# Kernel optimization log

Measured on AMD Instinct MI355X. Metric: run time of the kernel, lower is better.

## Reference

```python
import jax, jax.numpy as jnp
import numpy as np

B, C, HF, WF = 64, 512, 28, 28
HID = 512
NUM_CLS = 30
LOC_REG = 8
MAX_LEN = 500  # loop runs MAX_LEN + 1 = 501 steps


def setup_inputs() -> dict:
    key = jax.random.key(0)
    ks = jax.random.split(key, 12)
    sc = 0.02
    rn = lambda k, shape: jax.random.normal(k, shape, jnp.float32) * sc
    z = lambda shape: jnp.zeros(shape, jnp.float32)
    return {
        "fea": jax.random.normal(ks[0], (B, C, HF, WF), jnp.float32),
        # AttentionGRUCell params
        "i2h_w": rn(ks[1], (HID, C)),            # Linear(C, H, bias=False)
        "h2h_w": rn(ks[2], (HID, HID)),
        "h2h_b": z((HID,)),
        "score_w": rn(ks[3], (1, HID)),          # Linear(H, 1, bias=False)
        "gru_w_ih": rn(ks[4], (3 * HID, C + NUM_CLS)),
        "gru_w_hh": rn(ks[5], (3 * HID, HID)),
        "gru_b_ih": z((3 * HID,)),
        "gru_b_hh": z((3 * HID,)),
        # structure_generator: Linear(H,H) -> Linear(H, NUM_CLS) (no activation)
        "sg1_w": rn(ks[6], (HID, HID)), "sg1_b": z((HID,)),
        "sg2_w": rn(ks[7], (NUM_CLS, HID)), "sg2_b": z((NUM_CLS,)),
        # loc_generator: Linear(H,H) -> Linear(H, LOC_REG) -> Sigmoid
        "lg1_w": rn(ks[8], (HID, HID)), "lg1_b": z((HID,)),
        "lg2_w": rn(ks[9], (LOC_REG, HID)), "lg2_b": z((LOC_REG,)),
    }


def reference(fea, i2h_w, h2h_w, h2h_b, score_w, gru_w_ih, gru_w_hh,
              gru_b_ih, gru_b_hh, sg1_w, sg1_b, sg2_w, sg2_b,
              lg1_w, lg1_b, lg2_w, lg2_b):
    b = fea.shape[0]
    feat = fea.reshape(b, fea.shape[1], -1).transpose(0, 2, 1)      # [B, T, C]
    # i2h(batch_H) is step-invariant: hoist it out of the decode loop
    feat_proj = jnp.einsum('btc,hc->bth', feat, i2h_w)              # [B, T, H]
    sv = score_w[0]                                                  # [H]

    def gru_cell(x, h):
        gi = x @ gru_w_ih.T + gru_b_ih
        gh = h @ gru_w_hh.T + gru_b_hh
        i_r, i_z, i_n = jnp.split(gi, 3, axis=-1)
        h_r, h_z, h_n = jnp.split(gh, 3, axis=-1)
        r = jax.nn.sigmoid(i_r + h_r)
        z = jax.nn.sigmoid(i_z + h_z)
        n = jnp.tanh(i_n + r * h_n)
        return (1.0 - z) * n + z * h

    def step(carry, _):
        hidden, pre_chars = carry
        onehot = jax.nn.one_hot(pre_chars, NUM_CLS, dtype=feat.dtype)
        hproj = hidden @ h2h_w.T + h2h_b                             # [B, H]
        e = jnp.einsum('bth,h->bt', jnp.tanh(feat_proj + hproj[:, None, :]), sv)
        alpha = jax.nn.softmax(e, axis=1)                            # [B, T]
        context = jnp.einsum('bt,btc->bc', alpha, feat)              # [B, C]
        x = jnp.concatenate([context, onehot], axis=1)               # [B, C+NUM_CLS]
        new_hidden = gru_cell(x, hidden)
        structure_step = (new_hidden @ sg1_w.T + sg1_b) @ sg2_w.T + sg2_b
        loc_step = jax.nn.sigmoid((new_hidden @ lg1_w.T + lg1_b) @ lg2_w.T + lg2_b)
        new_chars = jnp.argmax(structure_step, axis=1)               # greedy decode
        return (new_hidden, new_chars), (structure_step, loc_step)

    hidden0 = jnp.zeros((b, HID), feat.dtype)
    chars0 = jnp.zeros((b,), jnp.int32)
    _, (structs, locs) = jax.lax.scan(step, (hidden0, chars0), None, length=MAX_LEN + 1)
    structure_probs = jax.nn.softmax(structs.transpose(1, 0, 2), axis=-1)  # eval-mode softmax
    loc_preds = locs.transpose(1, 0, 2)
    return structure_probs, loc_preds
```

## Files before the change

kernel.cpp:

```cpp
#include <hip/hip_runtime.h>
#include <hip/hip_bf16.h>


#define NB 64
#define TT 784
#define CC 512
#define HH 512
#define NCLS 30
#define LREG 8
#define STEPS 501
#define GRID_MAIN 256
#define THR_MAIN 1024

struct SlaP {
  __hip_bfloat16* feat16;
  __hip_bfloat16* fp16;
  float* hid2;
  float* hproj;
  float* h1sg;
  float* h1lg;
  float* ctx2;
  float* wsum;
  int*   chars;
  unsigned* bar;
  const float *score_w, *w_ih, *w_hh, *b_ih, *b_hh;
  const float *h2h_w, *h2h_b, *sg1_w, *sg1_b, *sg2_w, *sg2_b;
  const float *lg1_w, *lg1_b, *lg2_w, *lg2_b;
  float *out_probs, *out_loc;
};

__device__ __forceinline__ float lo16(unsigned v){ return __uint_as_float(v << 16); }
__device__ __forceinline__ float hi16(unsigned v){ return __uint_as_float(v & 0xffff0000u); }

__device__ __forceinline__ float cld(const float* p){
  return __hip_atomic_load(p, __ATOMIC_RELAXED, __HIP_MEMORY_SCOPE_AGENT);
}
__device__ __forceinline__ void cst(float* p, float v){
  __hip_atomic_store(p, v, __ATOMIC_RELAXED, __HIP_MEMORY_SCOPE_AGENT);
}
__device__ __forceinline__ int cldi(const int* p){
  return __hip_atomic_load(p, __ATOMIC_RELAXED, __HIP_MEMORY_SCOPE_AGENT);
}
__device__ __forceinline__ void csti(int* p, int v){
  __hip_atomic_store(p, v, __ATOMIC_RELAXED, __HIP_MEMORY_SCOPE_AGENT);
}
__device__ __forceinline__ float2 cld2(const float* p){
  unsigned long long v = __hip_atomic_load((const unsigned long long*)p,
                          __ATOMIC_RELAXED, __HIP_MEMORY_SCOPE_AGENT);
  union { unsigned long long u; float2 f; } c; c.u = v; return c.f;
}
__device__ __forceinline__ void cst2(float* p, float a, float b){
  union { unsigned long long u; float2 f; } c; c.f = make_float2(a, b);
  __hip_atomic_store((unsigned long long*)p, c.u,
                     __ATOMIC_RELAXED, __HIP_MEMORY_SCOPE_AGENT);
}

__device__ __forceinline__ float tanh_fast(float x){
  float ex = __expf(2.f * x);
  return 1.f - 2.f * __builtin_amdgcn_rcpf(ex + 1.f);
}
__device__ __forceinline__ float sigmoid_fast(float x){
  return __builtin_amdgcn_rcpf(1.f + __expf(-x));
}
__device__ __forceinline__ float warp_sum(float v){
  #pragma unroll
  for (int m = 32; m > 0; m >>= 1) v += __shfl_xor(v, m, 64);
  return v;
}
__device__ __forceinline__ void warp_sum2(float& a, float& b){
  #pragma unroll
  for (int m = 32; m > 0; m >>= 1){
    float ta = __shfl_xor(a, m, 64);
    float tb = __shfl_xor(b, m, 64);
    a += ta; b += tb;
  }
}
__device__ __forceinline__ float warp_max(float v){
  #pragma unroll
  for (int m = 32; m > 0; m >>= 1) v = fmaxf(v, __shfl_xor(v, m, 64));
  return v;
}
__device__ __forceinline__ int warp_min_i(int v){
  #pragma unroll
  for (int m = 32; m > 0; m >>= 1) v = min(v, __shfl_xor(v, m, 64));
  return v;
}

__device__ __forceinline__ void gbar(unsigned* bar, unsigned target){
  __syncthreads();
  if (threadIdx.x == 0){
    unsigned* c8 = bar + 8 + (blockIdx.x & 7) * 32;
    unsigned p = __hip_atomic_fetch_add(c8, 1u, __ATOMIC_RELAXED, __HIP_MEMORY_SCOPE_AGENT);
    if (p == 32u * target - 1u){
      unsigned pm = __hip_atomic_fetch_add(bar, 1u, __ATOMIC_RELAXED, __HIP_MEMORY_SCOPE_AGENT);
      if (pm == 8u * target - 1u)
        __hip_atomic_store(bar + 64, target, __ATOMIC_RELAXED, __HIP_MEMORY_SCOPE_AGENT);
    }
    while (__hip_atomic_load(bar + 64, __ATOMIC_RELAXED, __HIP_MEMORY_SCOPE_AGENT) < target)
      __builtin_amdgcn_s_sleep(1);
  }
  __syncthreads();
}


__global__ void k_init(SlaP p){
  int idx = blockIdx.x * blockDim.x + threadIdx.x;
  if (idx < 32768){ p.hid2[idx] = 0.f; p.ctx2[idx] = 0.f; }
  if (idx < 64*512) p.hproj[idx] = p.h2h_b[idx & 511];
  if (idx < 64){ p.wsum[idx] = 0.f; p.chars[idx] = 0; }
  if (idx < 512) p.bar[idx] = 0u;
}

__global__ void k_transpose(const float* __restrict__ fea, __hip_bfloat16* __restrict__ feat16){
  __shared__ float tile[64][65];
  const int b = blockIdx.z, t0 = blockIdx.x * 64, c0 = blockIdx.y * 64;
  #pragma unroll
  for (int r = 0; r < 16; ++r){
    int idx = threadIdx.x + 256*r;
    int ci = idx >> 6, tj = idx & 63;
    float v = 0.f;
    if (t0 + tj < TT) v = fea[((size_t)b*CC + (c0+ci))*TT + t0 + tj];
    tile[ci][tj] = v;
  }
  __syncthreads();
  #pragma unroll
  for (int r = 0; r < 16; ++r){
    int idx = threadIdx.x + 256*r;
    int tj = idx >> 6, ci = idx & 63;
    if (t0 + tj < TT)
      feat16[((size_t)b*TT + t0 + tj)*CC + c0 + ci] = __float2bfloat16(tile[ci][tj]);
  }
}

__global__ void k_fpgemm(const float* __restrict__ fea, const float* __restrict__ i2h,
                         __hip_bfloat16* __restrict__ fp16){
  const int b = blockIdx.z, t0 = blockIdx.x * 64, h0 = blockIdx.y * 64;
  const int tx = threadIdx.x & 15, ty = threadIdx.x >> 4;
  const int tb = t0 + tx*4, hb = h0 + ty*4;
  const int ts = (tb < TT) ? tb : 0;
  const float* A = fea + (size_t)b*CC*TT;
  float acc[4][4];
  #pragma unroll
  for (int j = 0; j < 4; ++j)
    #pragma unroll
    for (int i2 = 0; i2 < 4; ++i2) acc[j][i2] = 0.f;
  for (int k = 0; k < CC; ++k){
    const float4 a4 = *(const float4*)&A[(size_t)k*TT + ts];
    float bv0 = i2h[(size_t)(hb+0)*CC + k];
    float bv1 = i2h[(size_t)(hb+1)*CC + k];
    float bv2 = i2h[(size_t)(hb+2)*CC + k];
    float bv3 = i2h[(size_t)(hb+3)*CC + k];
    acc[0][0] += bv0*a4.x; acc[0][1] += bv0*a4.y; acc[0][2] += bv0*a4.z; acc[0][3] += bv0*a4.w;
    acc[1][0] += bv1*a4.x; acc[1][1] += bv1*a4.y; acc[1][2] += bv1*a4.z; acc[1][3] += bv1*a4.w;
    acc[2][0] += bv2*a4.x; acc[2][1] += bv2*a4.y; acc[2][2] += bv2*a4.z; acc[2][3] += bv2*a4.w;
    acc[3][0] += bv3*a4.x; acc[3][1] += bv3*a4.y; acc[3][2] += bv3*a4.z; acc[3][3] += bv3*a4.w;
  }
  if (tb < TT){
    #pragma unroll
    for (int j = 0; j < 4; ++j)
      #pragma unroll
      for (int i2 = 0; i2 < 4; ++i2)
        fp16[((size_t)b*TT + tb + i2)*CC + hb + j] = __float2bfloat16(acc[j][i2]);
  }
}


__global__ void __launch_bounds__(THR_MAIN, 4) sla_main(SlaP p){
  const int tid  = threadIdx.x;
  const int lane = tid & 63;
  const int wv   = tid >> 6;
  const int blk  = blockIdx.x;
  __shared__ float sm[12352];
  float* smF = sm + 12288;

  const int ab = blk >> 2;
  const int aslice = blk & 3;
  float svr[8];
  #pragma unroll
  for (int k = 0; k < 8; ++k) svr[k] = p.score_w[lane*8 + k];

  unsigned bid = 0;

  for (int i = 0; i <= STEPS; ++i){
    if (i > 0 && blk < NB){
      const int fb = blk;
      for (int task = wv; task < 38; task += 16){
        const float* wrow; const float* src; float bias;
        if (task < 30){ wrow = p.sg2_w + task*512; bias = p.sg2_b[task]; src = p.h1sg + fb*512; }
        else          { wrow = p.lg2_w + (task-30)*512; bias = p.lg2_b[task-30]; src = p.h1lg + fb*512; }
        float s = 0.f;
        #pragma unroll
        for (int kq = 0; kq < 4; ++kq){
          const float2 wv2 = *(const float2*)&wrow[lane*2 + 128*kq];
          const float2 sv2 = cld2(&src[lane*2 + 128*kq]);
          s += wv2.x*sv2.x + wv2.y*sv2.y;
        }
        s = warp_sum(s);
        if (task < 30){ if (lane == 0) smF[task] = s + bias; }
        else if (lane == 0)
          p.out_loc[(size_t)fb*(STEPS*LREG) + (size_t)(i-1)*LREG + (task-30)] = sigmoid_fast(s + bias);
      }
    }
    __syncthreads();
    if (i > 0 && blk < NB && wv == 0){
      float sv_ = (lane < 30) ? smF[lane] : -3.4e38f;
      float m = warp_max(sv_);
      float e = (lane < 30) ? __expf(sv_ - m) : 0.f;
      float ssum = warp_sum(e);
      if (lane < 30)
        p.out_probs[(size_t)blk*(STEPS*NCLS) + (size_t)(i-1)*NCLS + lane] = e / ssum;
      int cand = (lane < 30 && sv_ == m) ? lane : 1000;
      cand = warp_min_i(cand);
      if (lane == 0) csti(&p.chars[blk], cand);
    }
    if (i == STEPS) break;
    {
      float hpr[8];
      #pragma unroll
      for (int k = 0; k < 4; ++k){
        float2 h2 = cld2(&p.hproj[ab*512 + lane*8 + 2*k]);
        hpr[2*k] = h2.x; hpr[2*k+1] = h2.y;
      }
      float acc[8] = {0,0,0,0,0,0,0,0};
      float wsr = 0.f;
      const int tl0 = aslice * 196;
      const unsigned short* fpB = (const unsigned short*)p.fp16 + ((size_t)ab*TT)*512;
      const unsigned short* ftB = (const unsigned short*)p.feat16 + ((size_t)ab*TT)*512;
      const int cnt = (wv < 4) ? 13 : 12;
      const int r0r = wv*12 + ((wv < 4) ? wv : 4);
      const unsigned short* fpR = fpB + (size_t)(tl0 + r0r)*512 + lane*8;
      const unsigned short* ftR = ftB + (size_t)(tl0 + r0r)*512 + lane*8;
      uint4 f0 = *(const uint4*)(fpR);
      uint4 g0 = *(const uint4*)(ftR);
      uint4 f1 = *(const uint4*)(fpR + 512);
      uint4 g1 = *(const uint4*)(ftR + 512);
      const int np = cnt >> 1;
      for (int pi = 0; pi < np; ++pi){
        const uint4 cf0 = f0, cg0 = g0, cf1 = f1, cg1 = g1;
        fpR += 1024; ftR += 1024;
        if (pi + 1 < np){
          f0 = *(const uint4*)(fpR);       g0 = *(const uint4*)(ftR);
          f1 = *(const uint4*)(fpR + 512); g1 = *(const uint4*)(ftR + 512);
        } else if (cnt & 1){
          f0 = *(const uint4*)(fpR);       g0 = *(const uint4*)(ftR);
        }
        float ea = 0.f, eb = 0.f, x;
        x = lo16(cf0.x)+hpr[0]; ea += tanh_fast(x)*svr[0];
        x = lo16(cf1.x)+hpr[0]; eb += tanh_fast(x)*svr[0];
        x = hi16(cf0.x)+hpr[1]; ea += tanh_fast(x)*svr[1];
        x = hi16(cf1.x)+hpr[1]; eb += tanh_fast(x)*svr[1];
        x = lo16(cf0.y)+hpr[2]; ea += tanh_fast(x)*svr[2];
        x = lo16(cf1.y)+hpr[2]; eb += tanh_fast(x)*svr[2];
        x = hi16(cf0.y)+hpr[3]; ea += tanh_fast(x)*svr[3];
        x = hi16(cf1.y)+hpr[3]; eb += tanh_fast(x)*svr[3];
        x = lo16(cf0.z)+hpr[4]; ea += tanh_fast(x)*svr[4];
        x = lo16(cf1.z)+hpr[4]; eb += tanh_fast(x)*svr[4];
        x = hi16(cf0.z)+hpr[5]; ea += tanh_fast(x)*svr[5];
        x = hi16(cf1.z)+hpr[5]; eb += tanh_fast(x)*svr[5];
        x = lo16(cf0.w)+hpr[6]; ea += tanh_fast(x)*svr[6];
        x = lo16(cf1.w)+hpr[6]; eb += tanh_fast(x)*svr[6];
        x = hi16(cf0.w)+hpr[7]; ea += tanh_fast(x)*svr[7];
        x = hi16(cf1.w)+hpr[7]; eb += tanh_fast(x)*svr[7];
        warp_sum2(ea, eb);
        const float wa = __expf(ea), wb = __expf(eb);
        acc[0] += wa*lo16(cg0.x) + wb*lo16(cg1.x);
        acc[1] += wa*hi16(cg0.x) + wb*hi16(cg1.x);
        acc[2] += wa*lo16(cg0.y) + wb*lo16(cg1.y);
        acc[3] += wa*hi16(cg0.y) + wb*hi16(cg1.y);
        acc[4] += wa*lo16(cg0.z) + wb*lo16(cg1.z);
        acc[5] += wa*hi16(cg0.z) + wb*hi16(cg1.z);
        acc[6] += wa*lo16(cg0.w) + wb*lo16(cg1.w);
        acc[7] += wa*hi16(cg0.w) + wb*hi16(cg1.w);
        wsr += wa + wb;
      }
      if (cnt & 1){
        float e0 = 0.f, x;
        x = lo16(f0.x)+hpr[0]; e0 += tanh_fast(x)*svr[0];
        x = hi16(f0.x)+hpr[1]; e0 += tanh_fast(x)*svr[1];
        x = lo16(f0.y)+hpr[2]; e0 += tanh_fast(x)*svr[2];
        x = hi16(f0.y)+hpr[3]; e0 += tanh_fast(x)*svr[3];
        x = lo16(f0.z)+hpr[4]; e0 += tanh_fast(x)*svr[4];
        x = hi16(f0.z)+hpr[5]; e0 += tanh_fast(x)*svr[5];
        x = lo16(f0.w)+hpr[6]; e0 += tanh_fast(x)*svr[6];
        x = hi16(f0.w)+hpr[7]; e0 += tanh_fast(x)*svr[7];
        e0 = warp_sum(e0);
        const float wa = __expf(e0);
        acc[0] += wa*lo16(g0.x); acc[1] += wa*hi16(g0.x);
        acc[2] += wa*lo16(g0.y); acc[3] += wa*hi16(g0.y);
        acc[4] += wa*lo16(g0.z); acc[5] += wa*hi16(g0.z);
        acc[6] += wa*lo16(g0.w); acc[7] += wa*hi16(g0.w);
        wsr += wa;
      }
      if (wv < 8){
        #pragma unroll
        for (int k = 0; k < 8; ++k) sm[wv*512 + lane*8 + k] = acc[k];
      }
      if (lane == 0) smF[32 + wv] = wsr;
      __syncthreads();
      if (wv >= 8){
        #pragma unroll
        for (int k = 0; k < 8; ++k) sm[(wv-8)*512 + lane*8 + k] += acc[k];
      }
      __syncthreads();
      if (tid < 512){
        float s = 0.f;
        #pragma unroll
        for (int r = 0; r < 8; ++r) s += sm[r*512 + tid];
        unsafeAtomicAdd(&p.ctx2[(tid >> 1)*128 + ab*2 + (tid & 1)], s);
      } else if (tid == 512){
        float s = 0.f;
        #pragma unroll
        for (int r = 0; r < 16; ++r) s += smF[32 + r];
        unsafeAtomicAdd(&p.wsum[ab], s);
      }
    }
    gbar(p.bar, ++bid);
    if (blk < 128){
      const int j0 = blk * 4;
      const float* hidC = p.hid2 + (i & 1)*(512*64);
      float accI[4][3], accH[4][3];
      #pragma unroll
      for (int jj = 0; jj < 4; ++jj)
        #pragma unroll
        for (int g = 0; g < 3; ++g){ accI[jj][g] = 0.f; accH[jj][g] = 0.f; }
      const int kb = wv * 32;
      for (int kk = 0; kk < 32; kk += 4){
        const int k = kb + kk;
        const float2 x01 = cld2(&p.ctx2[(k >> 1)*128 + lane*2]);
        const float2 x23 = cld2(&p.ctx2[(k >> 1)*128 + 128 + lane*2]);
        const float2 h01 = cld2(&hidC[(k >> 1)*128 + lane*2]);
        const float2 h23 = cld2(&hidC[(k >> 1)*128 + 128 + lane*2]);
        #pragma unroll
        for (int jj = 0; jj < 4; ++jj)
          #pragma unroll
          for (int g = 0; g < 3; ++g){
            const int row = g*512 + j0 + jj;
            const float4 wi = *(const float4*)&p.w_ih[(size_t)row*542 + k];
            const float4 wh = *(const float4*)&p.w_hh[(size_t)row*512 + k];
            accI[jj][g] += wi.x*x01.x + wi.y*x01.y + wi.z*x23.x + wi.w*x23.y;
            accH[jj][g] += wh.x*h01.x + wh.y*h01.y + wh.z*h23.x + wh.w*h23.y;
          }
      }
      const int slot = wv & 7;
      if (wv < 8){
        #pragma unroll
        for (int jj = 0; jj < 4; ++jj)
          #pragma unroll
          for (int g = 0; g < 3; ++g){
            sm[((slot*24) + jj*6 + g    )*64 + lane] = accI[jj][g];
            sm[((slot*24) + jj*6 + 3 + g)*64 + lane] = accH[jj][g];
          }
      }
      __syncthreads();
      if (wv >= 8){
        #pragma unroll
        for (int jj = 0; jj < 4; ++jj)
          #pragma unroll
          for (int g = 0; g < 3; ++g){
            sm[((slot*24) + jj*6 + g    )*64 + lane] += accI[jj][g];
            sm[((slot*24) + jj*6 + 3 + g)*64 + lane] += accH[jj][g];
          }
      }
      __syncthreads();
      if (tid < 128){
        const int pp = tid >> 6;
        const int b = tid & 63;
        float ws = 0.f;
        ws = cld(&p.wsum[b]);
        const float inv = 1.f / ws;
        const int ch = cldi(&p.chars[b]);
        const float2 ho = cld2(&hidC[((j0 >> 1) + pp)*128 + b*2]);
        float nh[2];
        #pragma unroll
        for (int q = 0; q < 2; ++q){
          const int jj = pp*2 + q;
          float gi[3], gh[3];
          #pragma unroll
          for (int g = 0; g < 3; ++g){
            float giS = 0.f, ghS = 0.f;
            #pragma unroll
            for (int sl = 0; sl < 8; ++sl){
              giS += sm[((sl*24) + jj*6 + g    )*64 + b];
              ghS += sm[((sl*24) + jj*6 + 3 + g)*64 + b];
            }
            const int row = g*512 + j0 + jj;
            gi[g] = giS*inv + p.w_ih[(size_t)row*542 + 512 + ch] + p.b_ih[row];
            gh[g] = ghS + p.b_hh[row];
          }
          float r_ = sigmoid_fast(gi[0] + gh[0]);
          float z_ = sigmoid_fast(gi[1] + gh[1]);
          float n_ = tanh_fast(gi[2] + r_*gh[2]);
          float hold = (q == 0) ? ho.x : ho.y;
          nh[q] = (1.f - z_)*n_ + z_*hold;
        }
        cst2(&p.hid2[((i+1) & 1)*(512*64) + ((j0 >> 1) + pp)*128 + b*2], nh[0], nh[1]);
      }
    } else {
      __syncthreads(); __syncthreads();
    }
    gbar(p.bar, ++bid);
    if (blk < 128){
      const int r0 = blk * 12;
      const float* hidN = p.hid2 + ((i+1) & 1)*(512*64);
      const float* rowp[12];
      #pragma unroll
      for (int r = 0; r < 12; ++r){
        const int rg = r0 + r, head = rg >> 9, j = rg & 511;
        const float* base = (head == 0) ? p.h2h_w : (head == 1) ? p.sg1_w : p.lg1_w;
        rowp[r] = base + (size_t)j*512;
      }
      float acc[12];
      #pragma unroll
      for (int r = 0; r < 12; ++r) acc[r] = 0.f;
      const int kb = wv * 32;
      for (int kk = 0; kk < 32; kk += 4){
        const int k = kb + kk;
        const float2 h01 = cld2(&hidN[(k >> 1)*128 + lane*2]);
        const float2 h23 = cld2(&hidN[(k >> 1)*128 + 128 + lane*2]);
        #pragma unroll
        for (int r = 0; r < 12; ++r){
          const float4 w4 = *(const float4*)&rowp[r][k];
          acc[r] += w4.x*h01.x + w4.y*h01.y + w4.z*h23.x + w4.w*h23.y;
        }
      }
      const int slot = wv & 7;
      if (wv < 8){
        #pragma unroll
        for (int r = 0; r < 12; ++r) sm[((slot*12) + r)*64 + lane] = acc[r];
      }
      __syncthreads();
      if (wv >= 8){
        #pragma unroll
        for (int r = 0; r < 12; ++r) sm[((slot*12) + r)*64 + lane] += acc[r];
      }
      __syncthreads();
      if (tid < 384){
        const int q = tid >> 6, b = tid & 63;
        float s0 = 0.f, s1 = 0.f;
        #pragma unroll
        for (int sl = 0; sl < 8; ++sl){
          s0 += sm[((sl*12) + 2*q    )*64 + b];
          s1 += sm[((sl*12) + 2*q + 1)*64 + b];
        }
        const int rg = r0 + 2*q, head = rg >> 9, j = rg & 511;
        const float* bb = (head == 0) ? p.h2h_b : (head == 1) ? p.sg1_b : p.lg1_b;
        float* dst = (head == 0) ? p.hproj : (head == 1) ? p.h1sg : p.h1lg;
        cst2(&dst[b*512 + j], s0 + bb[j], s1 + bb[j+1]);
      }
    } else {
      const int bz = blk - 128;
      if (tid < 256) cst(&p.ctx2[bz*256 + tid], 0.f);
      if (bz == 127 && tid < 64) cst(&p.wsum[tid], 0.f);
      __syncthreads(); __syncthreads();
    }
    gbar(p.bar, ++bid);
  }
}

extern "C" void kernel_launch(void* const* d_in, const int* in_sizes, int n_in,
                              void* d_out, int out_size, void* d_ws, size_t ws_size,
                              hipStream_t stream){
  (void)in_sizes; (void)n_in; (void)out_size; (void)ws_size;
  char* w = (char*)d_ws;
  size_t off = 0;
  auto carve = [&](size_t bytes) -> char* {
    char* r = w + off; off += (bytes + 255) & ~(size_t)255; return r;
  };
  SlaP p;
  p.feat16 = (__hip_bfloat16*)carve((size_t)NB*TT*CC*2);
  p.fp16   = (__hip_bfloat16*)carve((size_t)NB*TT*HH*2);
  p.hid2   = (float*)carve((size_t)2*512*64*4);
  p.hproj  = (float*)carve((size_t)64*512*4);
  p.h1sg   = (float*)carve((size_t)64*512*4);
  p.h1lg   = (float*)carve((size_t)64*512*4);
  p.ctx2   = (float*)carve((size_t)512*64*4);
  p.wsum   = (float*)carve(64*4);
  p.chars  = (int*)carve(64*4);
  p.bar    = (unsigned*)carve(2048);

  p.score_w = (const float*)d_in[4];
  p.w_ih  = (const float*)d_in[5];  p.w_hh  = (const float*)d_in[6];
  p.b_ih  = (const float*)d_in[7];  p.b_hh  = (const float*)d_in[8];
  p.h2h_w = (const float*)d_in[2];  p.h2h_b = (const float*)d_in[3];
  p.sg1_w = (const float*)d_in[9];  p.sg1_b = (const float*)d_in[10];
  p.sg2_w = (const float*)d_in[11]; p.sg2_b = (const float*)d_in[12];
  p.lg1_w = (const float*)d_in[13]; p.lg1_b = (const float*)d_in[14];
  p.lg2_w = (const float*)d_in[15]; p.lg2_b = (const float*)d_in[16];
  p.out_probs = (float*)d_out;
  p.out_loc   = p.out_probs + (size_t)NB*STEPS*NCLS;

  const float* fea = (const float*)d_in[0];
  const float* i2h = (const float*)d_in[1];

  k_init<<<128, 256, 0, stream>>>(p);
  k_transpose<<<dim3(13, 8, 64), 256, 0, stream>>>(fea, p.feat16);
  k_fpgemm<<<dim3(13, 8, 64), 256, 0, stream>>>(fea, i2h, p.fp16);
  sla_main<<<GRID_MAIN, THR_MAIN, 0, stream>>>(p);
}
```

Baseline: 38.80 ms.

## Cache part of attention feature rows in LDS and batch four rows per reduction

```diff
diff --git a/kernel.cpp b/kernel.cpp
--- a/kernel.cpp
+++ b/kernel.cpp
@@ -11,6 +11,7 @@
 #define STEPS 501
 #define GRID_MAIN 256
 #define THR_MAIN 1024
+#define LROWS 52
 
 struct SlaP {
   __hip_bfloat16* feat16;
@@ -67,14 +68,6 @@
   for (int m = 32; m > 0; m >>= 1) v += __shfl_xor(v, m, 64);
   return v;
 }
-__device__ __forceinline__ void warp_sum2(float& a, float& b){
-  #pragma unroll
-  for (int m = 32; m > 0; m >>= 1){
-    float ta = __shfl_xor(a, m, 64);
-    float tb = __shfl_xor(b, m, 64);
-    a += ta; b += tb;
-  }
-}
 __device__ __forceinline__ float warp_max(float v){
   #pragma unroll
   for (int m = 32; m > 0; m >>= 1) v = fmaxf(v, __shfl_xor(v, m, 64));
@@ -84,6 +77,43 @@
   #pragma unroll
   for (int m = 32; m > 0; m >>= 1) v = min(v, __shfl_xor(v, m, 64));
   return v;
+}
+
+__device__ __forceinline__ void att_quad(const uint4* f, const uint4* g, int count,
+                                         const float* hpr, const float* svr,
+                                         float* acc, float& wsr){
+  float e[4];
+  #pragma unroll
+  for (int j = 0; j < 4; ++j){
+    float s = 0.f, x;
+    x = lo16(f[j].x)+hpr[0]; s += tanh_fast(x)*svr[0];
+    x = hi16(f[j].x)+hpr[1]; s += tanh_fast(x)*svr[1];
+    x = lo16(f[j].y)+hpr[2]; s += tanh_fast(x)*svr[2];
+    x = hi16(f[j].y)+hpr[3]; s += tanh_fast(x)*svr[3];
+    x = lo16(f[j].z)+hpr[4]; s += tanh_fast(x)*svr[4];
+    x = hi16(f[j].z)+hpr[5]; s += tanh_fast(x)*svr[5];
+    x = lo16(f[j].w)+hpr[6]; s += tanh_fast(x)*svr[6];
+    x = hi16(f[j].w)+hpr[7]; s += tanh_fast(x)*svr[7];
+    e[j] = s;
+  }
+  #pragma unroll
+  for (int m = 32; m > 0; m >>= 1){
+    e[0] += __shfl_xor(e[0], m, 64);
+    e[1] += __shfl_xor(e[1], m, 64);
+    e[2] += __shfl_xor(e[2], m, 64);
+    e[3] += __shfl_xor(e[3], m, 64);
+  }
+  float w[4];
+  #pragma unroll
+  for (int j = 0; j < 4; ++j) w[j] = (j < count) ? __expf(e[j]) : 0.f;
+  #pragma unroll
+  for (int j = 0; j < 4; ++j){
+    acc[0] += w[j]*lo16(g[j].x); acc[1] += w[j]*hi16(g[j].x);
+    acc[2] += w[j]*lo16(g[j].y); acc[3] += w[j]*hi16(g[j].y);
+    acc[4] += w[j]*lo16(g[j].z); acc[5] += w[j]*hi16(g[j].z);
+    acc[6] += w[j]*lo16(g[j].w); acc[7] += w[j]*hi16(g[j].w);
+    wsr += w[j];
+  }
 }
 
 __device__ __forceinline__ void gbar(unsigned* bar, unsigned target){
@@ -171,6 +201,8 @@
   const int wv   = tid >> 6;
   const int blk  = blockIdx.x;
   __shared__ float sm[12352];
+  __shared__ unsigned short lfp[LROWS*512];
+  __shared__ unsigned short lft[LROWS*512];
   float* smF = sm + 12288;
 
   const int ab = blk >> 2;
@@ -178,6 +210,10 @@
   float svr[8];
   #pragma unroll
   for (int k = 0; k < 8; ++k) svr[k] = p.score_w[lane*8 + k];
+
+  const int lbase = wv*3 + ((wv < 4) ? wv : 4);
+  const int lcnt  = (wv < 4) ? 4 : 3;
+  const int gbase = LROWS + wv*9;
 
   unsigned bid = 0;
 
@@ -224,73 +260,52 @@
       float acc[8] = {0,0,0,0,0,0,0,0};
       float wsr = 0.f;
       const int tl0 = aslice * 196;
-      const unsigned short* fpB = (const unsigned short*)p.fp16 + ((size_t)ab*TT)*512;
-      const unsigned short* ftB = (const unsigned short*)p.feat16 + ((size_t)ab*TT)*512;
-      const int cnt = (wv < 4) ? 13 : 12;
-      const int r0r = wv*12 + ((wv < 4) ? wv : 4);
-      const unsigned short* fpR = fpB + (size_t)(tl0 + r0r)*512 + lane*8;
-      const unsigned short* ftR = ftB + (size_t)(tl0 + r0r)*512 + lane*8;
-      uint4 f0 = *(const uint4*)(fpR);
-      uint4 g0 = *(const uint4*)(ftR);
-      uint4 f1 = *(const uint4*)(fpR + 512);
-      uint4 g1 = *(const uint4*)(ftR + 512);
-      const int np = cnt >> 1;
-      for (int pi = 0; pi < np; ++pi){
-        const uint4 cf0 = f0, cg0 = g0, cf1 = f1, cg1 = g1;
-        fpR += 1024; ftR += 1024;
-        if (pi + 1 < np){
-          f0 = *(const uint4*)(fpR);       g0 = *(const uint4*)(ftR);
-          f1 = *(const uint4*)(fpR + 512); g1 = *(const uint4*)(ftR + 512);
-        } else if (cnt & 1){
-          f0 = *(const uint4*)(fpR);       g0 = *(const uint4*)(ftR);
+      const unsigned short* fpB = (const unsigned short*)p.fp16 +
+                                  ((size_t)ab*TT + tl0)*512 + lane*8;
+      const unsigned short* ftB = (const unsigned short*)p.feat16 +
+                                  ((size_t)ab*TT + tl0)*512 + lane*8;
+      uint4 qf[2][4], qg[2][4];
+      #pragma unroll
+      for (int j = 0; j < 4; ++j){
+        qf[0][j] = *(const uint4*)(fpB + (size_t)(gbase+j)*512);
+        qg[0][j] = *(const uint4*)(ftB + (size_t)(gbase+j)*512);
+      }
+      #pragma unroll
+      for (int j = 0; j < 4; ++j){
+        qf[1][j] = *(const uint4*)(fpB + (size_t)(gbase+4+j)*512);
+        qg[1][j] = *(const uint4*)(ftB + (size_t)(gbase+4+j)*512);
+      }
+      {
+        uint4 lf[4], lg[4];
+        if (i == 0){
+          #pragma unroll
+          for (int j = 0; j < 4; ++j){
+            const int rj = lbase + ((j < lcnt) ? j : (lcnt-1));
+            lf[j] = *(const uint4*)(fpB + (size_t)rj*512);
+            lg[j] = *(const uint4*)(ftB + (size_t)rj*512);
+          }
+          #pragma unroll
+          for (int j = 0; j < 4; ++j){
+            if (j < lcnt){
+              *(uint4*)&lfp[(lbase+j)*512 + lane*8] = lf[j];
+              *(uint4*)&lft[(lbase+j)*512 + lane*8] = lg[j];
+            }
+          }
+        } else {
+          #pragma unroll
+          for (int j = 0; j < 4; ++j){
+            const int rj = lbase + ((j < lcnt) ? j : (lcnt-1));
+            lf[j] = *(const uint4*)&lfp[rj*512 + lane*8];
+            lg[j] = *(const uint4*)&lft[rj*512 + lane*8];
+          }
         }
-        float ea = 0.f, eb = 0.f, x;
-        x = lo16(cf0.x)+hpr[0]; ea += tanh_fast(x)*svr[0];
-        x = lo16(cf1.x)+hpr[0]; eb += tanh_fast(x)*svr[0];
-        x = hi16(cf0.x)+hpr[1]; ea += tanh_fast(x)*svr[1];
-        x = hi16(cf1.x)+hpr[1]; eb += tanh_fast(x)*svr[1];
-        x = lo16(cf0.y)+hpr[2]; ea += tanh_fast(x)*svr[2];
-        x = lo16(cf1.y)+hpr[2]; eb += tanh_fast(x)*svr[2];
-        x = hi16(cf0.y)+hpr[3]; ea += tanh_fast(x)*svr[3];
-        x = hi16(cf1.y)+hpr[3]; eb += tanh_fast(x)*svr[3];
-        x = lo16(cf0.z)+hpr[4]; ea += tanh_fast(x)*svr[4];
-        x = lo16(cf1.z)+hpr[4]; eb += tanh_fast(x)*svr[4];
-        x = hi16(cf0.z)+hpr[5]; ea += tanh_fast(x)*svr[5];
-        x = hi16(cf1.z)+hpr[5]; eb += tanh_fast(x)*svr[5];
-        x = lo16(cf0.w)+hpr[6]; ea += tanh_fast(x)*svr[6];
-        x = lo16(cf1.w)+hpr[6]; eb += tanh_fast(x)*svr[6];
-        x = hi16(cf0.w)+hpr[7]; ea += tanh_fast(x)*svr[7];
-        x = hi16(cf1.w)+hpr[7]; eb += tanh_fast(x)*svr[7];
-        warp_sum2(ea, eb);
-        const float wa = __expf(ea), wb = __expf(eb);
-        acc[0] += wa*lo16(cg0.x) + wb*lo16(cg1.x);
-        acc[1] += wa*hi16(cg0.x) + wb*hi16(cg1.x);
-        acc[2] += wa*lo16(cg0.y) + wb*lo16(cg1.y);
-        acc[3] += wa*hi16(cg0.y) + wb*hi16(cg1.y);
-        acc[4] += wa*lo16(cg0.z) + wb*lo16(cg1.z);
-        acc[5] += wa*hi16(cg0.z) + wb*hi16(cg1.z);
-        acc[6] += wa*lo16(cg0.w) + wb*lo16(cg1.w);
-        acc[7] += wa*hi16(cg0.w) + wb*hi16(cg1.w);
-        wsr += wa + wb;
-      }
-      if (cnt & 1){
-        float e0 = 0.f, x;
-        x = lo16(f0.x)+hpr[0]; e0 += tanh_fast(x)*svr[0];
-        x = hi16(f0.x)+hpr[1]; e0 += tanh_fast(x)*svr[1];
-        x = lo16(f0.y)+hpr[2]; e0 += tanh_fast(x)*svr[2];
-        x = hi16(f0.y)+hpr[3]; e0 += tanh_fast(x)*svr[3];
-        x = lo16(f0.z)+hpr[4]; e0 += tanh_fast(x)*svr[4];
-        x = hi16(f0.z)+hpr[5]; e0 += tanh_fast(x)*svr[5];
-        x = lo16(f0.w)+hpr[6]; e0 += tanh_fast(x)*svr[6];
-        x = hi16(f0.w)+hpr[7]; e0 += tanh_fast(x)*svr[7];
-        e0 = warp_sum(e0);
-        const float wa = __expf(e0);
-        acc[0] += wa*lo16(g0.x); acc[1] += wa*hi16(g0.x);
-        acc[2] += wa*lo16(g0.y); acc[3] += wa*hi16(g0.y);
-        acc[4] += wa*lo16(g0.z); acc[5] += wa*hi16(g0.z);
-        acc[6] += wa*lo16(g0.w); acc[7] += wa*hi16(g0.w);
-        wsr += wa;
-      }
+        att_quad(lf, lg, lcnt, hpr, svr, acc, wsr);
+      }
+      att_quad(qf[0], qg[0], 4, hpr, svr, acc, wsr);
+      qf[0][0] = *(const uint4*)(fpB + (size_t)(gbase+8)*512);
+      qg[0][0] = *(const uint4*)(ftB + (size_t)(gbase+8)*512);
+      att_quad(qf[1], qg[1], 4, hpr, svr, acc, wsr);
+      att_quad(qf[0], qg[0], 1, hpr, svr, acc, wsr);
       if (wv < 8){
         #pragma unroll
         for (int k = 0; k < 8; ++k) sm[wv*512 + lane*8 + k] = acc[k];
@@ -365,9 +380,7 @@
       if (tid < 128){
         const int pp = tid >> 6;
         const int b = tid & 63;
-        float ws = 0.f;
-        ws = cld(&p.wsum[b]);
-        const float inv = 1.f / ws;
+        const float inv = 1.f / cld(&p.wsum[b]);
         const int ch = cldi(&p.chars[b]);
         const float2 ho = cld2(&hidC[((j0 >> 1) + pp)*128 + b*2]);
         float nh[2];
```

Result: slower. 46.41 ms (+19.6%).
